# Performance work log

Measured on AMD Instinct MI355X. Metric: run time of the kernel, lower is better.

## Reference

```python
import jax, jax.numpy as jnp
import numpy as np

BLOCK_SIZE = 64

def quantize_dequantize(w, block_size=BLOCK_SIZE):
    # LPBQ double quantization: block-wise abs-max -> uint4 scale1 over fp32 scale2
    out_ch, in_ch = w.shape
    pad_len = (block_size - in_ch % block_size) % block_size
    if pad_len > 0:
        w = jnp.pad(w, ((0, 0), (0, pad_len)))
    wr = w.reshape(out_ch, -1, block_size)                      # [O, nB, B]
    s1 = jnp.clip(jnp.max(jnp.abs(wr), axis=-1, keepdims=True) / 7.0, 1e-8)   # [O, nB, 1]
    s2 = jnp.clip(jnp.max(s1, axis=1, keepdims=True) / 15.0, 1e-8)            # [O, 1, 1]
    s1_q = jnp.clip(jnp.round(s1 / s2), 0.0, 15.0)
    s1_recon = s1_q * s2
    w_q = jnp.clip(jnp.round(wr / s1_recon), -8.0, 7.0)
    w_recon = (w_q * s1_recon).reshape(out_ch, -1)
    if pad_len > 0:
        w_recon = w_recon[:, :-pad_len]
    return w_recon

def setup_inputs() -> dict:
    key = jax.random.key(0)
    k1, k2, k3 = jax.random.split(key, 3)
    B, S, IN, OUT = 1, 128, 4096, 11008
    x = jax.random.normal(k1, (B, S, IN), dtype=jnp.float32)
    weight = jax.random.normal(k2, (OUT, IN), dtype=jnp.float32)
    bias = jax.random.normal(k3, (OUT,), dtype=jnp.float32)
    return {"x": x, "weight": weight, "bias": bias}

def reference(x, weight, bias):
    w_q = quantize_dequantize(weight)
    # F.linear: x @ w_q.T + bias
    return jnp.einsum('bsi,oi->bso', x, w_q) + bias
```

## Files before the change

kernel.cpp:

```cpp
#include <hip/hip_runtime.h>
#include <hip/hip_bf16.h>

#define IN_CH 4096
#define OUT_CH 11008
#define QBLK 64

#define BM 128
#define BN 64
#define BK 64
#define KCHUNKS (IN_CH / BK)
#define XCONV_BLOCKS 16

typedef short bf16x8 __attribute__((ext_vector_type(8)));
typedef float f32x4 __attribute__((ext_vector_type(4)));

#define GLOBAL_AS __attribute__((address_space(1)))
#define LDS_AS __attribute__((address_space(3)))

__device__ inline unsigned short f2bf(float f) {
    union { __hip_bfloat16 h; unsigned short u; } cv;
    cv.h = __float2bfloat16(f);
    return cv.u;
}

__global__ __launch_bounds__(256) void quant_kernel(
        const float* __restrict__ w, const float* __restrict__ x,
        unsigned short* __restrict__ wq, unsigned short* __restrict__ xq) {
    const int tid = threadIdx.x;

    if (blockIdx.x >= OUT_CH) {
        const int bx = blockIdx.x - OUT_CH;
        const float4* x4 = (const float4*)x;
        for (int it = 0; it < 32; ++it) {
            const int g = bx * 8192 + it * 256 + tid;
            float4 v = x4[g];
            ushort4 o;
            o.x = f2bf(v.x); o.y = f2bf(v.y); o.z = f2bf(v.z); o.w = f2bf(v.w);
            ((ushort4*)xq)[g] = o;
        }
        return;
    }

    const float* wrow = w + (size_t)blockIdx.x * IN_CH;
    unsigned short* orow = wq + (size_t)blockIdx.x * IN_CH;

    __shared__ float s1_lds[64];
    __shared__ float s2_lds;

    float4 v[4];
    const int lane16 = tid & 15;

    for (int p = 0; p < 4; ++p) {
        v[p] = ((const float4*)wrow)[p * 256 + tid];
        float m = fmaxf(fmaxf(fabsf(v[p].x), fabsf(v[p].y)),
                        fmaxf(fabsf(v[p].z), fabsf(v[p].w)));
        m = fmaxf(m, __shfl_xor(m, 1));
        m = fmaxf(m, __shfl_xor(m, 2));
        m = fmaxf(m, __shfl_xor(m, 4));
        m = fmaxf(m, __shfl_xor(m, 8));
        if (lane16 == 0)
            s1_lds[p * 16 + (tid >> 4)] = fmaxf(m * (1.0f / 7.0f), 1e-8f);
    }
    __syncthreads();

    if (tid < 64) {
        float m = s1_lds[tid];
        m = fmaxf(m, __shfl_xor(m, 1));
        m = fmaxf(m, __shfl_xor(m, 2));
        m = fmaxf(m, __shfl_xor(m, 4));
        m = fmaxf(m, __shfl_xor(m, 8));
        m = fmaxf(m, __shfl_xor(m, 16));
        m = fmaxf(m, __shfl_xor(m, 32));
        if (tid == 0) s2_lds = fmaxf(m * (1.0f / 15.0f), 1e-8f);
    }
    __syncthreads();
    const float s2 = s2_lds;

    for (int p = 0; p < 4; ++p) {
        const float s1 = s1_lds[p * 16 + (tid >> 4)];
        const float s1q = fminf(fmaxf(rintf(s1 / s2), 0.0f), 15.0f);
        const float s1r = s1q * s2;
        ushort4 o;
        o.x = f2bf(fminf(fmaxf(rintf(v[p].x / s1r), -8.0f), 7.0f) * s1r);
        o.y = f2bf(fminf(fmaxf(rintf(v[p].y / s1r), -8.0f), 7.0f) * s1r);
        o.z = f2bf(fminf(fmaxf(rintf(v[p].z / s1r), -8.0f), 7.0f) * s1r);
        o.w = f2bf(fminf(fmaxf(rintf(v[p].w / s1r), -8.0f), 7.0f) * s1r);
        ((ushort4*)orow)[p * 256 + tid] = o;
    }
}

__global__ __launch_bounds__(256) void gemm_kernel(
        const unsigned short* __restrict__ A, const unsigned short* __restrict__ B,
        const float* __restrict__ bias, float* __restrict__ C) {
    __shared__ __align__(16) unsigned short ldsA[BM * BK];
    __shared__ __align__(16) unsigned short ldsB[BN * BK];

    const int tid = threadIdx.x;
    const int w = tid >> 6;
    const int l = tid & 63;
    const int wm = w >> 1;
    const int wn = w & 1;
    const int n0 = blockIdx.x * BN;

    const int r8 = l >> 3;
    const int sg = l & 7;

    f32x4 acc[4][2] = {};

    const int lane15 = l & 15;
    const int quad = l >> 4;

    for (int kc = 0; kc < KCHUNKS; ++kc) {
        const int k0 = kc * BK;

        for (int i = 0; i < 4; ++i) {
            const int r = i * 32 + w * 8 + r8;
            const unsigned short* gp = A + (size_t)r * IN_CH + k0 + sg * 8;
            LDS_AS unsigned short* lp =
                (LDS_AS unsigned short*)&ldsA[(i * 32 + w * 8) * BK];
            __builtin_amdgcn_global_load_lds((const GLOBAL_AS void*)gp,
                                             (LDS_AS void*)lp, 16, 0, 0);
        }
        for (int j = 0; j < 2; ++j) {
            const int r = j * 32 + w * 8 + r8;
            const unsigned short* gp = B + (size_t)(n0 + r) * IN_CH + k0 + sg * 8;
            LDS_AS unsigned short* lp =
                (LDS_AS unsigned short*)&ldsB[(j * 32 + w * 8) * BK];
            __builtin_amdgcn_global_load_lds((const GLOBAL_AS void*)gp,
                                             (LDS_AS void*)lp, 16, 0, 0);
        }
        asm volatile("s_waitcnt vmcnt(0)" ::: "memory");
        __syncthreads();

        for (int kk = 0; kk < 2; ++kk) {
            bf16x8 af[4], bfv[2];
            const int ko = kk * 32 + quad * 8;
            for (int i = 0; i < 4; ++i)
                af[i] = *(const bf16x8*)&ldsA[(wm * 64 + i * 16 + lane15) * BK + ko];
            for (int j = 0; j < 2; ++j)
                bfv[j] = *(const bf16x8*)&ldsB[(wn * 32 + j * 16 + lane15) * BK + ko];
            for (int i = 0; i < 4; ++i)
                for (int j = 0; j < 2; ++j)
                    acc[i][j] = __builtin_amdgcn_mfma_f32_16x16x32_bf16(
                        af[i], bfv[j], acc[i][j], 0, 0, 0);
        }
        __syncthreads();
    }

    const int m_base = wm * 64 + quad * 4;
    const int n_base = n0 + wn * 32 + lane15;
    for (int j = 0; j < 2; ++j) {
        const float bv = bias[n_base + j * 16];
        for (int i = 0; i < 4; ++i) {
            const int m = m_base + i * 16;
            float* cp = C + (size_t)m * OUT_CH + n_base + j * 16;
            cp[0 * OUT_CH] = acc[i][j][0] + bv;
            cp[1 * OUT_CH] = acc[i][j][1] + bv;
            cp[2 * OUT_CH] = acc[i][j][2] + bv;
            cp[3 * OUT_CH] = acc[i][j][3] + bv;
        }
    }
}

extern "C" void kernel_launch(void* const* d_in, const int* in_sizes, int n_in,
                              void* d_out, int out_size, void* d_ws, size_t ws_size,
                              hipStream_t stream) {
    const float* x = (const float*)d_in[0];
    const float* weight = (const float*)d_in[1];
    const float* bias = (const float*)d_in[2];
    float* out = (float*)d_out;

    unsigned short* wsW = (unsigned short*)d_ws;
    unsigned short* wsX = wsW + (size_t)OUT_CH * IN_CH;

    quant_kernel<<<OUT_CH + XCONV_BLOCKS, 256, 0, stream>>>(weight, x, wsW, wsX);
    gemm_kernel<<<OUT_CH / BN, 256, 0, stream>>>(wsX, wsW, bias, out);
}
```

Before: 329.8 us.

## Split GEMM over K into four partial slices with separate bias-reduce kernel

The GEMM grid gains a second dimension that splits the K loop into four slices, each writing fp32 partial sums to workspace. A new reduce kernel sums the partials and adds the bias. This raises the block count well above the CU count so more of the GPU is busy. In exchange it adds extra partial-sum traffic and a third kernel launch.

```diff
diff --git a/kernel.cpp b/kernel.cpp
--- a/kernel.cpp
+++ b/kernel.cpp
@@ -9,6 +9,9 @@
 #define BN 64
 #define BK 64
 #define KCHUNKS (IN_CH / BK)
+#define KSPLIT 4
+#define SPLIT_CHUNKS (KCHUNKS / KSPLIT)
+#define NTILES (OUT_CH / BN)
 #define XCONV_BLOCKS 16
 
 typedef short bf16x8 __attribute__((ext_vector_type(8)));
@@ -91,7 +94,7 @@
 
 __global__ __launch_bounds__(256) void gemm_kernel(
         const unsigned short* __restrict__ A, const unsigned short* __restrict__ B,
-        const float* __restrict__ bias, float* __restrict__ C) {
+        float* __restrict__ part) {
     __shared__ __align__(16) unsigned short ldsA[BM * BK];
     __shared__ __align__(16) unsigned short ldsB[BN * BK];
 
@@ -101,6 +104,7 @@
     const int wm = w >> 1;
     const int wn = w & 1;
     const int n0 = blockIdx.x * BN;
+    const int kc0 = blockIdx.y * SPLIT_CHUNKS;
 
     const int r8 = l >> 3;
     const int sg = l & 7;
@@ -110,7 +114,7 @@
     const int lane15 = l & 15;
     const int quad = l >> 4;
 
-    for (int kc = 0; kc < KCHUNKS; ++kc) {
+    for (int kc = kc0; kc < kc0 + SPLIT_CHUNKS; ++kc) {
         const int k0 = kc * BK;
 
         for (int i = 0; i < 4; ++i) {
@@ -147,19 +151,35 @@
         __syncthreads();
     }
 
+    float* pbase = part + (size_t)blockIdx.y * BM * OUT_CH;
     const int m_base = wm * 64 + quad * 4;
     const int n_base = n0 + wn * 32 + lane15;
     for (int j = 0; j < 2; ++j) {
-        const float bv = bias[n_base + j * 16];
         for (int i = 0; i < 4; ++i) {
             const int m = m_base + i * 16;
-            float* cp = C + (size_t)m * OUT_CH + n_base + j * 16;
-            cp[0 * OUT_CH] = acc[i][j][0] + bv;
-            cp[1 * OUT_CH] = acc[i][j][1] + bv;
-            cp[2 * OUT_CH] = acc[i][j][2] + bv;
-            cp[3 * OUT_CH] = acc[i][j][3] + bv;
-        }
-    }
+            float* cp = pbase + (size_t)m * OUT_CH + n_base + j * 16;
+            cp[0 * OUT_CH] = acc[i][j][0];
+            cp[1 * OUT_CH] = acc[i][j][1];
+            cp[2 * OUT_CH] = acc[i][j][2];
+            cp[3 * OUT_CH] = acc[i][j][3];
+        }
+    }
+}
+
+__global__ __launch_bounds__(256) void reduce_kernel(
+        const float* __restrict__ part, const float* __restrict__ bias,
+        float* __restrict__ out) {
+    const int m = blockIdx.y;
+    const int x4 = blockIdx.x * 256 + threadIdx.x;
+    if (x4 >= OUT_CH / 4) return;
+    const size_t off = (size_t)m * OUT_CH + x4 * 4;
+
+    float4 acc = ((const float4*)bias)[x4];
+    for (int s = 0; s < KSPLIT; ++s) {
+        float4 p = *(const float4*)(part + (size_t)s * BM * OUT_CH + off);
+        acc.x += p.x; acc.y += p.y; acc.z += p.z; acc.w += p.w;
+    }
+    *(float4*)(out + off) = acc;
 }
 
 extern "C" void kernel_launch(void* const* d_in, const int* in_sizes, int n_in,
@@ -172,7 +192,10 @@
 
     unsigned short* wsW = (unsigned short*)d_ws;
     unsigned short* wsX = wsW + (size_t)OUT_CH * IN_CH;
+    float* wsP = (float*)(wsX + (size_t)BM * IN_CH);
 
     quant_kernel<<<OUT_CH + XCONV_BLOCKS, 256, 0, stream>>>(weight, x, wsW, wsX);
-    gemm_kernel<<<OUT_CH / BN, 256, 0, stream>>>(wsX, wsW, bias, out);
-}
+    gemm_kernel<<<dim3(NTILES, KSPLIT), 256, 0, stream>>>(wsX, wsW, wsP);
+    reduce_kernel<<<dim3((OUT_CH / 4 + 255) / 256, BM), 256, 0, stream>>>(
+        wsP, bias, out);
+}
```

After: 300.8 us. 1.1x faster.

## Fuse weight quantize-dequantize into GEMM and drop bf16 weight workspace

Applied to the files above, without the earlier changes.

The weight quantization pass is folded into the GEMM kernel. Each block first scans its 32 weight rows to compute per-block and per-row scales in LDS. It then quantizes fp32 weight tiles on the fly into padded LDS while the next tile is prefetched into registers. This removes the write and re-read of an 90 MB bf16 weight copy, but each block now reads its fp32 weights twice. BN is halved to 32, which doubles the grid to 344 blocks and doubles the number of times activation tiles are re-read.

```diff
diff --git a/kernel.cpp b/kernel.cpp
--- a/kernel.cpp
+++ b/kernel.cpp
@@ -3,13 +3,13 @@
 
 #define IN_CH 4096
 #define OUT_CH 11008
-#define QBLK 64
 
 #define BM 128
-#define BN 64
+#define BN 32
 #define BK 64
 #define KCHUNKS (IN_CH / BK)
-#define XCONV_BLOCKS 16
+#define NBLOCKS (OUT_CH / BN)
+#define BPAD 72
 
 typedef short bf16x8 __attribute__((ext_vector_type(8)));
 typedef float f32x4 __attribute__((ext_vector_type(4)));
@@ -23,123 +23,114 @@
     return cv.u;
 }
 
-__global__ __launch_bounds__(256) void quant_kernel(
-        const float* __restrict__ w, const float* __restrict__ x,
-        unsigned short* __restrict__ wq, unsigned short* __restrict__ xq) {
+__global__ __launch_bounds__(256) void xconv_kernel(
+        const float* __restrict__ x, unsigned short* __restrict__ xq) {
     const int tid = threadIdx.x;
+    const float4* x4 = (const float4*)x;
+    for (int it = 0; it < 32; ++it) {
+        const int g = blockIdx.x * 8192 + it * 256 + tid;
+        float4 v = x4[g];
+        ushort4 o;
+        o.x = f2bf(v.x); o.y = f2bf(v.y); o.z = f2bf(v.z); o.w = f2bf(v.w);
+        ((ushort4*)xq)[g] = o;
+    }
+}
 
-    if (blockIdx.x >= OUT_CH) {
-        const int bx = blockIdx.x - OUT_CH;
-        const float4* x4 = (const float4*)x;
-        for (int it = 0; it < 32; ++it) {
-            const int g = bx * 8192 + it * 256 + tid;
-            float4 v = x4[g];
-            ushort4 o;
-            o.x = f2bf(v.x); o.y = f2bf(v.y); o.z = f2bf(v.z); o.w = f2bf(v.w);
-            ((ushort4*)xq)[g] = o;
+__global__ __launch_bounds__(256) void fused_kernel(
+        const float* __restrict__ w, const unsigned short* __restrict__ xq,
+        const float* __restrict__ bias, float* __restrict__ out) {
+    __shared__ float s1r[BN * KCHUNKS];
+    __shared__ __align__(16) unsigned short ldsA[BM * BK];
+    __shared__ __align__(16) unsigned short ldsB[BN * BPAD];
+
+    const int tid = threadIdx.x;
+    const int n0 = blockIdx.x * BN;
+
+    {
+        const int kb = tid >> 2;
+        const int q4 = tid & 3;
+        for (int it = 0; it < BN; ++it) {
+            const float4* p =
+                (const float4*)(w + (size_t)(n0 + it) * IN_CH + kb * 64 + q4 * 16);
+            float4 a = p[0], b = p[1], c = p[2], d = p[3];
+            float m = fmaxf(
+                fmaxf(fmaxf(fmaxf(fabsf(a.x), fabsf(a.y)), fmaxf(fabsf(a.z), fabsf(a.w))),
+                      fmaxf(fmaxf(fabsf(b.x), fabsf(b.y)), fmaxf(fabsf(b.z), fabsf(b.w)))),
+                fmaxf(fmaxf(fmaxf(fabsf(c.x), fabsf(c.y)), fmaxf(fabsf(c.z), fabsf(c.w))),
+                      fmaxf(fmaxf(fabsf(d.x), fabsf(d.y)), fmaxf(fabsf(d.z), fabsf(d.w)))));
+            m = fmaxf(m, __shfl_xor(m, 1));
+            m = fmaxf(m, __shfl_xor(m, 2));
+            if (q4 == 0)
+                s1r[it * KCHUNKS + kb] = fmaxf(m * (1.0f / 7.0f), 1e-8f);
         }
-        return;
-    }
+        __syncthreads();
 
-    const float* wrow = w + (size_t)blockIdx.x * IN_CH;
-    unsigned short* orow = wq + (size_t)blockIdx.x * IN_CH;
-
-    __shared__ float s1_lds[64];
-    __shared__ float s2_lds;
-
-    float4 v[4];
-    const int lane16 = tid & 15;
-
-    for (int p = 0; p < 4; ++p) {
-        v[p] = ((const float4*)wrow)[p * 256 + tid];
-        float m = fmaxf(fmaxf(fabsf(v[p].x), fabsf(v[p].y)),
-                        fmaxf(fabsf(v[p].z), fabsf(v[p].w)));
+        const int row = tid >> 3;
+        const int j8 = tid & 7;
+        float v[8];
+        float m = 0.0f;
+        for (int t = 0; t < 8; ++t) {
+            v[t] = s1r[row * KCHUNKS + j8 * 8 + t];
+            m = fmaxf(m, v[t]);
+        }
         m = fmaxf(m, __shfl_xor(m, 1));
         m = fmaxf(m, __shfl_xor(m, 2));
         m = fmaxf(m, __shfl_xor(m, 4));
-        m = fmaxf(m, __shfl_xor(m, 8));
-        if (lane16 == 0)
-            s1_lds[p * 16 + (tid >> 4)] = fmaxf(m * (1.0f / 7.0f), 1e-8f);
+        const float s2 = fmaxf(m * (1.0f / 15.0f), 1e-8f);
+        for (int t = 0; t < 8; ++t) {
+            const float s1q = fminf(fmaxf(rintf(v[t] / s2), 0.0f), 15.0f);
+            s1r[row * KCHUNKS + j8 * 8 + t] = s1q * s2;
+        }
+        __syncthreads();
     }
-    __syncthreads();
 
-    if (tid < 64) {
-        float m = s1_lds[tid];
-        m = fmaxf(m, __shfl_xor(m, 1));
-        m = fmaxf(m, __shfl_xor(m, 2));
-        m = fmaxf(m, __shfl_xor(m, 4));
-        m = fmaxf(m, __shfl_xor(m, 8));
-        m = fmaxf(m, __shfl_xor(m, 16));
-        m = fmaxf(m, __shfl_xor(m, 32));
-        if (tid == 0) s2_lds = fmaxf(m * (1.0f / 15.0f), 1e-8f);
-    }
-    __syncthreads();
-    const float s2 = s2_lds;
+    const int w4 = tid >> 6, l = tid & 63;
+    const int r8 = l >> 3, sg = l & 7;
+    const int brow = tid >> 3, bseg = tid & 7;
+    const int lane15 = l & 15, quad = l >> 4;
 
-    for (int p = 0; p < 4; ++p) {
-        const float s1 = s1_lds[p * 16 + (tid >> 4)];
-        const float s1q = fminf(fmaxf(rintf(s1 / s2), 0.0f), 15.0f);
-        const float s1r = s1q * s2;
-        ushort4 o;
-        o.x = f2bf(fminf(fmaxf(rintf(v[p].x / s1r), -8.0f), 7.0f) * s1r);
-        o.y = f2bf(fminf(fmaxf(rintf(v[p].y / s1r), -8.0f), 7.0f) * s1r);
-        o.z = f2bf(fminf(fmaxf(rintf(v[p].z / s1r), -8.0f), 7.0f) * s1r);
-        o.w = f2bf(fminf(fmaxf(rintf(v[p].w / s1r), -8.0f), 7.0f) * s1r);
-        ((ushort4*)orow)[p * 256 + tid] = o;
-    }
-}
+    f32x4 acc[2][2] = {};
 
-__global__ __launch_bounds__(256) void gemm_kernel(
-        const unsigned short* __restrict__ A, const unsigned short* __restrict__ B,
-        const float* __restrict__ bias, float* __restrict__ C) {
-    __shared__ __align__(16) unsigned short ldsA[BM * BK];
-    __shared__ __align__(16) unsigned short ldsB[BN * BK];
-
-    const int tid = threadIdx.x;
-    const int w = tid >> 6;
-    const int l = tid & 63;
-    const int wm = w >> 1;
-    const int wn = w & 1;
-    const int n0 = blockIdx.x * BN;
-
-    const int r8 = l >> 3;
-    const int sg = l & 7;
-
-    f32x4 acc[4][2] = {};
-
-    const int lane15 = l & 15;
-    const int quad = l >> 4;
+    const float* wrow = w + (size_t)(n0 + brow) * IN_CH + bseg * 8;
+    float4 c0 = *(const float4*)(wrow);
+    float4 c1 = *(const float4*)(wrow + 4);
 
     for (int kc = 0; kc < KCHUNKS; ++kc) {
-        const int k0 = kc * BK;
-
         for (int i = 0; i < 4; ++i) {
-            const int r = i * 32 + w * 8 + r8;
-            const unsigned short* gp = A + (size_t)r * IN_CH + k0 + sg * 8;
+            const unsigned short* gp =
+                xq + (size_t)(i * 32 + w4 * 8 + r8) * IN_CH + kc * 64 + sg * 8;
             LDS_AS unsigned short* lp =
-                (LDS_AS unsigned short*)&ldsA[(i * 32 + w * 8) * BK];
+                (LDS_AS unsigned short*)&ldsA[(i * 32 + w4 * 8) * BK];
             __builtin_amdgcn_global_load_lds((const GLOBAL_AS void*)gp,
                                              (LDS_AS void*)lp, 16, 0, 0);
         }
-        for (int j = 0; j < 2; ++j) {
-            const int r = j * 32 + w * 8 + r8;
-            const unsigned short* gp = B + (size_t)(n0 + r) * IN_CH + k0 + sg * 8;
-            LDS_AS unsigned short* lp =
-                (LDS_AS unsigned short*)&ldsB[(j * 32 + w * 8) * BK];
-            __builtin_amdgcn_global_load_lds((const GLOBAL_AS void*)gp,
-                                             (LDS_AS void*)lp, 16, 0, 0);
+
+        const float s1 = s1r[brow * KCHUNKS + kc];
+        {
+            float fv[8] = {c0.x, c0.y, c0.z, c0.w, c1.x, c1.y, c1.z, c1.w};
+            bf16x8 ob;
+            for (int t = 0; t < 8; ++t) {
+                const float q = fminf(fmaxf(rintf(fv[t] / s1), -8.0f), 7.0f);
+                ob[t] = (short)f2bf(q * s1);
+            }
+            *(bf16x8*)&ldsB[brow * BPAD + bseg * 8] = ob;
         }
-        asm volatile("s_waitcnt vmcnt(0)" ::: "memory");
+
         __syncthreads();
 
+        if (kc + 1 < KCHUNKS) {
+            c0 = *(const float4*)(wrow + (kc + 1) * 64);
+            c1 = *(const float4*)(wrow + (kc + 1) * 64 + 4);
+        }
+
         for (int kk = 0; kk < 2; ++kk) {
-            bf16x8 af[4], bfv[2];
             const int ko = kk * 32 + quad * 8;
-            for (int i = 0; i < 4; ++i)
-                af[i] = *(const bf16x8*)&ldsA[(wm * 64 + i * 16 + lane15) * BK + ko];
-            for (int j = 0; j < 2; ++j)
-                bfv[j] = *(const bf16x8*)&ldsB[(wn * 32 + j * 16 + lane15) * BK + ko];
-            for (int i = 0; i < 4; ++i)
+            bf16x8 af[2], bfv[2];
+            af[0] = *(const bf16x8*)&ldsA[(w4 * 32 + lane15) * BK + ko];
+            af[1] = *(const bf16x8*)&ldsA[(w4 * 32 + 16 + lane15) * BK + ko];
+            bfv[0] = *(const bf16x8*)&ldsB[lane15 * BPAD + ko];
+            bfv[1] = *(const bf16x8*)&ldsB[(16 + lane15) * BPAD + ko];
+            for (int i = 0; i < 2; ++i)
                 for (int j = 0; j < 2; ++j)
                     acc[i][j] = __builtin_amdgcn_mfma_f32_16x16x32_bf16(
                         af[i], bfv[j], acc[i][j], 0, 0, 0);
@@ -147,13 +138,12 @@
         __syncthreads();
     }
 
-    const int m_base = wm * 64 + quad * 4;
-    const int n_base = n0 + wn * 32 + lane15;
+    const int m_base = w4 * 32 + quad * 4;
     for (int j = 0; j < 2; ++j) {
-        const float bv = bias[n_base + j * 16];
-        for (int i = 0; i < 4; ++i) {
-            const int m = m_base + i * 16;
-            float* cp = C + (size_t)m * OUT_CH + n_base + j * 16;
+        const int n = n0 + j * 16 + lane15;
+        const float bv = bias[n];
+        for (int i = 0; i < 2; ++i) {
+            float* cp = out + (size_t)(m_base + i * 16) * OUT_CH + n;
             cp[0 * OUT_CH] = acc[i][j][0] + bv;
             cp[1 * OUT_CH] = acc[i][j][1] + bv;
             cp[2 * OUT_CH] = acc[i][j][2] + bv;
@@ -170,9 +160,8 @@
     const float* bias = (const float*)d_in[2];
     float* out = (float*)d_out;
 
-    unsigned short* wsW = (unsigned short*)d_ws;
-    unsigned short* wsX = wsW + (size_t)OUT_CH * IN_CH;
+    unsigned short* wsX = (unsigned short*)d_ws;
 
-    quant_kernel<<<OUT_CH + XCONV_BLOCKS, 256, 0, stream>>>(weight, x, wsW, wsX);
-    gemm_kernel<<<OUT_CH / BN, 256, 0, stream>>>(wsX, wsW, bias, out);
+    xconv_kernel<<<16, 256, 0, stream>>>(x, wsX);
+    fused_kernel<<<NBLOCKS, 256, 0, stream>>>(weight, wsX, bias, out);
 }
```

Result: slower. 343.5 us (+4.2%).
